# Kernel tuning notes

Hardware: AMD Instinct MI355X
Metric: run time of the kernel (lower is better)

## Reference

```python
import jax, jax.numpy as jnp
import numpy as np

MARGIN = 0.5  # stands in for c.embedding_loss['margin']


def setup_inputs() -> dict:
    key = jax.random.key(0)
    k1, k2 = jax.random.split(key)
    emb = jax.random.normal(k1, (4, 64, 64, 64), dtype=jnp.float32)  # Bs x Ch x W x H
    lab = jax.random.randint(k2, (4, 64, 64), 0, 10)                 # Bs x W x H int labels
    return {"emb": emb, "lab": lab}


def reference(emb, lab):
    bs, ch, w, h = emb.shape
    N = h * w
    # Faithful to torch: input[i].view(h*w, ch) is a raw row-major reshape of [ch,w,h]
    E = emb.reshape(bs, N, ch)                     # [B, N, C]
    sim = jnp.einsum('bnc,bmc->bnm', E, E)         # cosine-sim-style Gram matrix [B,N,N]

    labf = lab.reshape(bs, N)
    same = labf[:, :, None] == labf[:, None, :]    # [B,N,N] bool; label_pair==+1 where same

    # pre-weight: 1 / (#pixels with same label) per pixel; count via pairwise equality
    counts = jnp.sum(same, axis=-1).astype(emb.dtype)   # [B,N]
    pw = 1.0 / counts
    weight = pw[:, :, None] * pw[:, None, :]            # [B,N,N] outer product per batch

    # positive pairs: 1 - sim ; negative pairs: relu(sim - margin)
    per_pair = jnp.where(same, 1.0 - sim, jnp.maximum(sim - MARGIN, 0.0))

    S = jnp.sum(weight * per_pair, axis=(1, 2))         # [B]
    # Original assigns the per-batch scalar (1/N)*S_i to an NxN tensor then sums everything:
    # total = sum_i N^2 * (1/N) * S_i = N * sum_i S_i
    return jnp.asarray(N, emb.dtype) * jnp.sum(S)
```

## Files before the change

### kernel.cpp

```cpp
#include <hip/hip_runtime.h>
#include <hip/hip_bf16.h>

#define NB    4
#define NPIX  4096
#define CH    64
#define TILE  128
#define TPB   32
#define PAIRS 528
#define MARGIN 0.5f

typedef __attribute__((ext_vector_type(8))) short   bf16x8;
typedef __attribute__((ext_vector_type(4))) float   f32x4;

static __device__ inline unsigned short f2bf(float x) {
    unsigned int u = __builtin_bit_cast(unsigned int, x);
    u = (u + 0x7FFFu + ((u >> 16) & 1u)) >> 16;
    return (unsigned short)u;
}

__global__ void prep_kernel(const int* __restrict__ lab, float* __restrict__ pw) {
    __shared__ int hist[16];
    int b = blockIdx.x;
    if (threadIdx.x < 16) hist[threadIdx.x] = 0;
    __syncthreads();
    const int* lb = lab + b * NPIX;
    for (int i = threadIdx.x; i < NPIX; i += 256) atomicAdd(&hist[lb[i]], 1);
    __syncthreads();
    float* pwb = pw + b * NPIX;
    for (int i = threadIdx.x; i < NPIX; i += 256) pwb[i] = 1.0f / (float)hist[lb[i]];
}

__launch_bounds__(256)
__global__ void pair_kernel(const float* __restrict__ emb, const int* __restrict__ lab,
                            const float* __restrict__ pw, float* __restrict__ partials) {
    __shared__ short As[TILE * CH];
    __shared__ short Bs[TILE * CH];
    __shared__ int   rlab[TILE], clab[TILE];
    __shared__ float rpw[TILE], cpw[TILE];
    __shared__ float wred[4];

    const int bid = blockIdx.x;
    const int b   = bid / PAIRS;
    int p = bid - b * PAIRS;
    int ti = 0, off = 0;
    while (p >= off + (TPB - ti)) { off += TPB - ti; ++ti; }
    const int tj = ti + (p - off);
    const int rowbase = ti * TILE, colbase = tj * TILE;

    const float* Eb = emb + (size_t)b * NPIX * CH;
    const int t = threadIdx.x;

    if (t < TILE) {
        rlab[t] = lab[b * NPIX + rowbase + t];
        rpw[t]  = pw[b * NPIX + rowbase + t];
    } else {
        int u = t - TILE;
        clab[u] = lab[b * NPIX + colbase + u];
        cpw[u]  = pw[b * NPIX + colbase + u];
    }

    {
        const int row  = t >> 1;
        const int half = t & 1;
        const float* srcA = Eb + (size_t)(rowbase + row) * CH + half * 32;
        const float* srcB = Eb + (size_t)(colbase + row) * CH + half * 32;
        char* AsB = (char*)As;
        char* BsB = (char*)Bs;
        const int sw = (row & 7) << 4;
#pragma unroll
        for (int j = 0; j < 4; ++j) {
            const int boff = row * 128 + ((half * 64 + j * 16) ^ sw);
            {
                f32x4 x0 = *(const f32x4*)(srcA + j * 8);
                f32x4 x1 = *(const f32x4*)(srcA + j * 8 + 4);
                union { bf16x8 v; unsigned short h[8]; } u;
#pragma unroll
                for (int e = 0; e < 4; ++e) { u.h[e] = f2bf(x0[e]); u.h[4 + e] = f2bf(x1[e]); }
                *(bf16x8*)(AsB + boff) = u.v;
            }
            {
                f32x4 x0 = *(const f32x4*)(srcB + j * 8);
                f32x4 x1 = *(const f32x4*)(srcB + j * 8 + 4);
                union { bf16x8 v; unsigned short h[8]; } u;
#pragma unroll
                for (int e = 0; e < 4; ++e) { u.h[e] = f2bf(x0[e]); u.h[4 + e] = f2bf(x1[e]); }
                *(bf16x8*)(BsB + boff) = u.v;
            }
        }
    }
    __syncthreads();

    const int lane = t & 63, wid = t >> 6;
    const int wr = wid >> 1, wc = wid & 1;
    const int lrow = lane & 15, lk = lane >> 4;

    f32x4 acc[4][4];
#pragma unroll
    for (int i = 0; i < 4; ++i)
#pragma unroll
        for (int j = 0; j < 4; ++j) acc[i][j] = (f32x4){0.f, 0.f, 0.f, 0.f};

    const char* AsB = (const char*)As;
    const char* BsB = (const char*)Bs;
#pragma unroll
    for (int kk = 0; kk < 2; ++kk) {
        bf16x8 af[4], bfv[4];
#pragma unroll
        for (int i = 0; i < 4; ++i) {
            const int row = wr * 64 + i * 16 + lrow;
            af[i] = *(const bf16x8*)(AsB + row * 128 + ((kk * 64 + lk * 16) ^ ((row & 7) << 4)));
        }
#pragma unroll
        for (int j = 0; j < 4; ++j) {
            const int row = wc * 64 + j * 16 + lrow;
            bfv[j] = *(const bf16x8*)(BsB + row * 128 + ((kk * 64 + lk * 16) ^ ((row & 7) << 4)));
        }
#pragma unroll
        for (int i = 0; i < 4; ++i)
#pragma unroll
            for (int j = 0; j < 4; ++j)
                acc[i][j] = __builtin_amdgcn_mfma_f32_16x16x32_bf16(af[i], bfv[j], acc[i][j], 0, 0, 0);
    }

    float facc = 0.f;
#pragma unroll
    for (int j = 0; j < 4; ++j) {
        const int c = wc * 64 + j * 16 + lrow;
        const int cl = clab[c];
        const float cp = cpw[c];
#pragma unroll
        for (int i = 0; i < 4; ++i) {
#pragma unroll
            for (int r = 0; r < 4; ++r) {
                const int rr = wr * 64 + i * 16 + lk * 4 + r;
                const float sim = acc[i][j][r];
                const float val = (rlab[rr] == cl) ? (1.0f - sim)
                                                   : fmaxf(sim - MARGIN, 0.0f);
                facc = fmaf(rpw[rr] * cp, val, facc);
            }
        }
    }

#pragma unroll
    for (int o = 32; o > 0; o >>= 1) facc += __shfl_down(facc, o);
    if (lane == 0) wred[wid] = facc;
    __syncthreads();
    if (t == 0) {
        float s = wred[0] + wred[1] + wred[2] + wred[3];
        partials[bid] = s * ((ti == tj) ? 1.0f : 2.0f);
    }
}

__global__ void reduce_kernel(const float* __restrict__ partials, float* __restrict__ out, int n) {
    float s = 0.f;
    for (int i = threadIdx.x; i < n; i += 256) s += partials[i];
#pragma unroll
    for (int o = 32; o > 0; o >>= 1) s += __shfl_down(s, o);
    __shared__ float wred[4];
    if ((threadIdx.x & 63) == 0) wred[threadIdx.x >> 6] = s;
    __syncthreads();
    if (threadIdx.x == 0) out[0] = (wred[0] + wred[1] + wred[2] + wred[3]) * (float)NPIX;
}

extern "C" void kernel_launch(void* const* d_in, const int* in_sizes, int n_in,
                              void* d_out, int out_size, void* d_ws, size_t ws_size,
                              hipStream_t stream) {
    const float* emb = (const float*)d_in[0];
    const int*   lab = (const int*)d_in[1];
    float* out = (float*)d_out;
    float* pw       = (float*)d_ws;
    float* partials = (float*)((char*)d_ws + NB * NPIX * sizeof(float));

    prep_kernel<<<NB, 256, 0, stream>>>(lab, pw);
    pair_kernel<<<NB * PAIRS, 256, 0, stream>>>(emb, lab, pw, partials);
    reduce_kernel<<<1, 256, 0, stream>>>(partials, out, NB * PAIRS);
}
```

Before: 88.39 us.

## Fuse label histogram into pair kernel and use packed bf16 conversion

Removes the separate prep kernel by having every pair block recompute the per-batch label histogram with wave ballots over all 4096 labels, then derive the pixel weights in shared memory. It also replaces the manual round-to-nearest-even bf16 conversion with the hardware v_cvt_pk_bf16_f32 instruction. This saves one kernel launch and a global round trip for the weights, but adds redundant histogram work in each of 2112 blocks (16 loads plus 160 ballots per thread). It also hardcodes the assumption of 10 label classes.

Measured after the change: 104.0 us. +17.7%, slower.

```diff
diff --git a/kernel.cpp b/kernel.cpp
--- a/kernel.cpp
+++ b/kernel.cpp
@@ -8,35 +8,26 @@
 #define TPB   32
 #define PAIRS 528
 #define MARGIN 0.5f
+#define NCLS  10
 
 typedef __attribute__((ext_vector_type(8))) short   bf16x8;
 typedef __attribute__((ext_vector_type(4))) float   f32x4;
+typedef __attribute__((ext_vector_type(4))) int     i32x4;
 
-static __device__ inline unsigned short f2bf(float x) {
-    unsigned int u = __builtin_bit_cast(unsigned int, x);
-    u = (u + 0x7FFFu + ((u >> 16) & 1u)) >> 16;
-    return (unsigned short)u;
-}
-
-__global__ void prep_kernel(const int* __restrict__ lab, float* __restrict__ pw) {
-    __shared__ int hist[16];
-    int b = blockIdx.x;
-    if (threadIdx.x < 16) hist[threadIdx.x] = 0;
-    __syncthreads();
-    const int* lb = lab + b * NPIX;
-    for (int i = threadIdx.x; i < NPIX; i += 256) atomicAdd(&hist[lb[i]], 1);
-    __syncthreads();
-    float* pwb = pw + b * NPIX;
-    for (int i = threadIdx.x; i < NPIX; i += 256) pwb[i] = 1.0f / (float)hist[lb[i]];
+static __device__ inline int cvt_pk_bf16(float lo, float hi) {
+    int r;
+    asm("v_cvt_pk_bf16_f32 %0, %1, %2" : "=v"(r) : "v"(lo), "v"(hi));
+    return r;
 }
 
 __launch_bounds__(256)
 __global__ void pair_kernel(const float* __restrict__ emb, const int* __restrict__ lab,
-                            const float* __restrict__ pw, float* __restrict__ partials) {
+                            float* __restrict__ partials) {
     __shared__ short As[TILE * CH];
     __shared__ short Bs[TILE * CH];
     __shared__ int   rlab[TILE], clab[TILE];
     __shared__ float rpw[TILE], cpw[TILE];
+    __shared__ int   histw[4][NCLS];
     __shared__ float wred[4];
 
     const int bid = blockIdx.x;
@@ -48,15 +39,26 @@
     const int rowbase = ti * TILE, colbase = tj * TILE;
 
     const float* Eb = emb + (size_t)b * NPIX * CH;
+    const int*   Lb = lab + b * NPIX;
     const int t = threadIdx.x;
+    const int lane = t & 63, wid = t >> 6;
 
-    if (t < TILE) {
-        rlab[t] = lab[b * NPIX + rowbase + t];
-        rpw[t]  = pw[b * NPIX + rowbase + t];
-    } else {
-        int u = t - TILE;
-        clab[u] = lab[b * NPIX + colbase + u];
-        cpw[u]  = pw[b * NPIX + colbase + u];
+    if (t < TILE) rlab[t] = Lb[rowbase + t];
+    else          clab[t - TILE] = Lb[colbase + (t - TILE)];
+
+    {
+        int cnt = 0;
+        const int* base = Lb + wid * 1024 + lane;
+#pragma unroll
+        for (int it = 0; it < 16; ++it) {
+            const int lv = base[it * 64];
+#pragma unroll
+            for (int c = 0; c < NCLS; ++c) {
+                unsigned long long m = __ballot(lv == c);
+                if (lane == c) cnt += (int)__popcll(m);
+            }
+        }
+        if (lane < NCLS) histw[wid][lane] = cnt;
     }
 
     {
@@ -73,24 +75,30 @@
             {
                 f32x4 x0 = *(const f32x4*)(srcA + j * 8);
                 f32x4 x1 = *(const f32x4*)(srcA + j * 8 + 4);
-                union { bf16x8 v; unsigned short h[8]; } u;
-#pragma unroll
-                for (int e = 0; e < 4; ++e) { u.h[e] = f2bf(x0[e]); u.h[4 + e] = f2bf(x1[e]); }
-                *(bf16x8*)(AsB + boff) = u.v;
+                i32x4 v = { cvt_pk_bf16(x0[0], x0[1]), cvt_pk_bf16(x0[2], x0[3]),
+                            cvt_pk_bf16(x1[0], x1[1]), cvt_pk_bf16(x1[2], x1[3]) };
+                *(i32x4*)(AsB + boff) = v;
             }
             {
                 f32x4 x0 = *(const f32x4*)(srcB + j * 8);
                 f32x4 x1 = *(const f32x4*)(srcB + j * 8 + 4);
-                union { bf16x8 v; unsigned short h[8]; } u;
-#pragma unroll
-                for (int e = 0; e < 4; ++e) { u.h[e] = f2bf(x0[e]); u.h[4 + e] = f2bf(x1[e]); }
-                *(bf16x8*)(BsB + boff) = u.v;
+                i32x4 v = { cvt_pk_bf16(x0[0], x0[1]), cvt_pk_bf16(x0[2], x0[3]),
+                            cvt_pk_bf16(x1[0], x1[1]), cvt_pk_bf16(x1[2], x1[3]) };
+                *(i32x4*)(BsB + boff) = v;
             }
         }
     }
     __syncthreads();
 
-    const int lane = t & 63, wid = t >> 6;
+    if (t < TILE) {
+        const int c = rlab[t];
+        rpw[t] = 1.0f / (float)(histw[0][c] + histw[1][c] + histw[2][c] + histw[3][c]);
+    } else {
+        const int u = t - TILE;
+        const int c = clab[u];
+        cpw[u] = 1.0f / (float)(histw[0][c] + histw[1][c] + histw[2][c] + histw[3][c]);
+    }
+
     const int wr = wid >> 1, wc = wid & 1;
     const int lrow = lane & 15, lk = lane >> 4;
 
@@ -121,6 +129,7 @@
             for (int j = 0; j < 4; ++j)
                 acc[i][j] = __builtin_amdgcn_mfma_f32_16x16x32_bf16(af[i], bfv[j], acc[i][j], 0, 0, 0);
     }
+    __syncthreads();
 
     float facc = 0.f;
 #pragma unroll
@@ -168,10 +177,8 @@
     const float* emb = (const float*)d_in[0];
     const int*   lab = (const int*)d_in[1];
     float* out = (float*)d_out;
-    float* pw       = (float*)d_ws;
-    float* partials = (float*)((char*)d_ws + NB * NPIX * sizeof(float));
+    float* partials = (float*)d_ws;
 
-    prep_kernel<<<NB, 256, 0, stream>>>(lab, pw);
-    pair_kernel<<<NB * PAIRS, 256, 0, stream>>>(emb, lab, pw, partials);
+    pair_kernel<<<NB * PAIRS, 256, 0, stream>>>(emb, lab, partials);
     reduce_kernel<<<1, 256, 0, stream>>>(partials, out, NB * PAIRS);
 }
```
